# Kernel optimization log

Hardware: AMD Instinct MI355X
Metric: run time of the kernel (lower is better)

Reference implementation:

```python
import jax, jax.numpy as jnp
import numpy as np

B, S, D_IN, D_OUT = 8, 2048, 768, 768
SCALE = float(D_IN) ** 0.5  # module divides by embed_size**0.5 where embed_size = input_dim


def setup_inputs() -> dict:
    key = jax.random.key(0)
    ks = jax.random.split(key, 8)
    std = 1.0 / np.sqrt(D_IN)
    return {
        "x": jax.random.normal(ks[0], (B, S, D_IN), dtype=jnp.float32),
        "mask": jax.random.randint(ks[1], (B, S), 0, 2, dtype=jnp.int32),
        "Wq": jax.random.normal(ks[2], (D_OUT, D_IN), dtype=jnp.float32) * std,
        "bq": jax.random.normal(ks[3], (D_OUT,), dtype=jnp.float32) * std,
        "Wk": jax.random.normal(ks[4], (D_OUT, D_IN), dtype=jnp.float32) * std,
        "bk": jax.random.normal(ks[5], (D_OUT,), dtype=jnp.float32) * std,
        "Wv": jax.random.normal(ks[6], (D_OUT, D_IN), dtype=jnp.float32) * std,
        "bv": jax.random.normal(ks[7], (D_OUT,), dtype=jnp.float32) * std,
    }


def reference(x, mask, Wq, bq, Wk, bk, Wv, bv):
    # QKV projections: nn.Linear computes x @ W.T + b
    Q = jnp.einsum("bsd,od->bso", x, Wq) + bq  # [B,S,D_OUT]
    K = jnp.einsum("bsd,od->bso", x, Wk) + bk
    V = jnp.einsum("bsd,od->bso", x, Wv) + bv
    scores = jnp.einsum("bqo,bko->bqk", Q, K) / SCALE  # [B,S,S]
    # key-position mask broadcast over query dim
    scores = jnp.where(mask[:, None, :] == 0, -jnp.inf, scores)
    weights = jax.nn.softmax(scores, axis=-1)
    out = jnp.einsum("bqk,bko->bqo", weights, V)  # [B,S,D_OUT]
    return out.mean(axis=1, keepdims=True)  # [B,1,D_OUT]
```

## Files before the change

### kernel.cpp

```cpp
#include <hip/hip_runtime.h>
#include <hip/hip_bf16.h>


#define S 2048
#define DIM 768
#define BATCH 8

typedef __hip_bfloat16 bf16;
typedef __attribute__((ext_vector_type(8))) short bf16x8;
typedef __attribute__((ext_vector_type(4))) short short4v;
typedef __attribute__((ext_vector_type(4))) float f32x4;

__device__ __forceinline__ f32x4 mfma16(bf16x8 a, bf16x8 b, f32x4 c) {
  return __builtin_amdgcn_mfma_f32_16x16x32_bf16(a, b, c, 0, 0, 0);
}

__device__ __forceinline__ void load_lds16(const short* g, short* l) {
  __builtin_amdgcn_global_load_lds(
      (const __attribute__((address_space(1))) unsigned int*)g,
      (__attribute__((address_space(3))) unsigned int*)l, 16, 0, 0);
}

__device__ __forceinline__ float b2f(short u) {
  union { float f; unsigned u; } v;
  v.u = ((unsigned)(unsigned short)u) << 16;
  return v.f;
}

__device__ __forceinline__ short f2b(float f) {
  bf16 h = __float2bfloat16(f);
  return *(short*)&h;
}

#define INV_SCALE 0.03608439182435161f

__global__ __launch_bounds__(256) void detect_dtype(const unsigned short* __restrict__ x,
                                                    int* __restrict__ flag) {
  int bad = 0;
  for (int i = threadIdx.x; i < 2048; i += 256) {
    int e = (x[i] >> 7) & 0xFF;
    if (e < 0x60 || e >= 0x9F) bad = 1;
  }
  if (bad) atomicOr(flag, 1);
}

__global__ __launch_bounds__(256) void prep_kernel(const void* __restrict__ Wq_raw,
                                                   const void* __restrict__ Wk_raw,
                                                   const void* __restrict__ bq_raw,
                                                   bf16* __restrict__ T0,
                                                   bf16* __restrict__ T1,
                                                   float* __restrict__ bvec,
                                                   const int* __restrict__ flag) {
  const int f = *flag;
  const int bx = blockIdx.x;
  if (bx < 288) {
    __shared__ unsigned short tile[64][66];
    const int p = bx / 144, r = bx % 144;
    const void* src = p ? Wk_raw : Wq_raw;
    unsigned short* dst = (unsigned short*)(p ? T1 : T0);
    const int obase = (r / 12) * 64, ibase = (r % 12) * 64;
    const int col = threadIdx.x & 63, rq = threadIdx.x >> 6;
#pragma unroll
    for (int rr = 0; rr < 64; rr += 4) {
      const long idx = (long)(obase + rr + rq) * DIM + ibase + col;
      const float v = f ? ((const float*)src)[idx] : b2f(((const short*)src)[idx]);
      tile[rr + rq][col] = (unsigned short)f2b(v);
    }
    __syncthreads();
#pragma unroll
    for (int rr = 0; rr < 64; rr += 4)
      dst[(long)(ibase + rr + rq) * DIM + obase + col] = tile[col][rr + rq];
  } else {
    const int o0 = (bx - 288) * 128;
    const int t = threadIdx.x;
    float s0 = 0.f, s1 = 0.f, s2 = 0.f;
    if (f) {
      const float* W = (const float*)Wk_raw;
      const float* bq = (const float*)bq_raw;
      for (int o = o0; o < o0 + 128; ++o) {
        const float bo = bq[o];
        const float* row = W + (long)o * DIM;
        s0 += row[t] * bo;
        s1 += row[t + 256] * bo;
        s2 += row[t + 512] * bo;
      }
    } else {
      const short* W = (const short*)Wk_raw;
      const short* bq = (const short*)bq_raw;
      for (int o = o0; o < o0 + 128; ++o) {
        const float bo = b2f(bq[o]);
        const short* row = W + (long)o * DIM;
        s0 += b2f(row[t]) * bo;
        s1 += b2f(row[t + 256]) * bo;
        s2 += b2f(row[t + 512]) * bo;
      }
    }
    atomicAdd(&bvec[t], s0);
    atomicAdd(&bvec[t + 256], s1);
    atomicAdd(&bvec[t + 512], s2);
  }
}

#define TILE_DECLS                                                          \
  __shared__ short As[4096], Bs[4096];                                      \
  const int tid = threadIdx.x;                                              \
  const int wave = tid >> 6, lane = tid & 63;                               \
  const int lr = lane & 15, quad = lane >> 4;                               \
  const int wm = (wave >> 1) * 64, wn = (wave & 1) * 64;                    \
  const int c0row = tid >> 2, colw = (tid & 3) * 8;

#define TILE_KLOOP(Abase, Bbase)                                            \
  const short* Ag0 = (Abase) + (long)(mblk + c0row) * DIM + colw;           \
  const short* Ag1 = (Abase) + (long)(mblk + 64 + c0row) * DIM + colw;      \
  const short* Bg0 = (Bbase) + (long)(nblk + c0row) * DIM + colw;           \
  const short* Bg1 = (Bbase) + (long)(nblk + 64 + c0row) * DIM + colw;      \
  short* Al0 = As + tid * 8;                                                \
  short* Al1 = As + 2048 + tid * 8;                                         \
  short* Bl0 = Bs + tid * 8;                                                \
  short* Bl1 = Bs + 2048 + tid * 8;                                         \
  f32x4 acc[4][4] = {};                                                     \
  for (int k0 = 0; k0 < DIM; k0 += 32) {                                    \
    load_lds16(Ag0 + k0, Al0);                                              \
    load_lds16(Ag1 + k0, Al1);                                              \
    load_lds16(Bg0 + k0, Bl0);                                              \
    load_lds16(Bg1 + k0, Bl1);                                              \
    asm volatile("s_waitcnt vmcnt(0)" ::: "memory");                        \
    __syncthreads();                                                        \
    bf16x8 af[4], bfr[4];                                                   \
    _Pragma("unroll") for (int it = 0; it < 4; ++it)                        \
        af[it] = *(const bf16x8*)(As + (wm + it * 16 + lr) * 32 + quad * 8);\
    _Pragma("unroll") for (int jt = 0; jt < 4; ++jt)                        \
        bfr[jt] = *(const bf16x8*)(Bs + (wn + jt * 16 + lr) * 32 + quad * 8);\
    _Pragma("unroll") for (int it = 0; it < 4; ++it)                        \
        _Pragma("unroll") for (int jt = 0; jt < 4; ++jt)                    \
            acc[it][jt] = mfma16(af[it], bfr[jt], acc[it][jt]);             \
    __syncthreads();                                                        \
  }

__global__ __launch_bounds__(256) void gemm_nt_tiled(const bf16* __restrict__ A,
                                                     const bf16* __restrict__ B,
                                                     bf16* __restrict__ D) {
  const int mblk = blockIdx.x * 128, nblk = blockIdx.y * 128;
  TILE_DECLS
  TILE_KLOOP((const short*)A, (const short*)B)
#pragma unroll
  for (int it = 0; it < 4; ++it)
#pragma unroll
    for (int jt = 0; jt < 4; ++jt)
#pragma unroll
      for (int r = 0; r < 4; ++r)
        D[(long)(mblk + wm + it * 16 + quad * 4 + r) * DIM +
          nblk + wn + jt * 16 + lr] = __float2bfloat16(acc[it][jt][r]);
}

__global__ __launch_bounds__(256) void mt_convert(const bf16* __restrict__ WkT,
                                                  const bf16* __restrict__ WqT,
                                                  bf16* __restrict__ Mt,
                                                  const void* __restrict__ x_raw,
                                                  const int* __restrict__ mask,
                                                  const float* __restrict__ bvec,
                                                  bf16* __restrict__ xb,
                                                  float* __restrict__ betas,
                                                  const int* __restrict__ flag) {
  const int bx = blockIdx.x;
  if (bx < 36) {
    const int mblk = (bx / 6) * 128, nblk = (bx % 6) * 128;
    TILE_DECLS
    TILE_KLOOP((const short*)WkT, (const short*)WqT)
#pragma unroll
    for (int it = 0; it < 4; ++it)
#pragma unroll
      for (int jt = 0; jt < 4; ++jt)
#pragma unroll
        for (int r = 0; r < 4; ++r)
          Mt[(long)(mblk + wm + it * 16 + quad * 4 + r) * DIM +
             nblk + wn + jt * 16 + lr] = __float2bfloat16(acc[it][jt][r]);
  } else {
    const int wave = threadIdx.x >> 6, lane = threadIdx.x & 63;
    const int n = (bx - 36) * 4 + wave;
    const int f = *flag;
    short* xo = (short*)xb + (long)n * DIM;
    float s = 0.f;
    if (f) {
      const float4* x4 = (const float4*)((const float*)x_raw + (long)n * DIM);
      const float4* bv4 = (const float4*)bvec;
#pragma unroll
      for (int it = 0; it < 3; ++it) {
        const int idx = it * 64 + lane;
        const float4 v = x4[idx];
        const float4 bb = bv4[idx];
        short4v sv = {f2b(v.x), f2b(v.y), f2b(v.z), f2b(v.w)};
        *(short4v*)(xo + idx * 4) = sv;
        s += v.x * bb.x + v.y * bb.y + v.z * bb.z + v.w * bb.w;
      }
    } else {
      const short4v* x4 = (const short4v*)((const short*)x_raw + (long)n * DIM);
      const float4* bv4 = (const float4*)bvec;
#pragma unroll
      for (int it = 0; it < 3; ++it) {
        const int idx = it * 64 + lane;
        const short4v v = x4[idx];
        const float4 bb = bv4[idx];
        *(short4v*)(xo + idx * 4) = v;
        s += b2f(v.x) * bb.x + b2f(v.y) * bb.y + b2f(v.z) * bb.z + b2f(v.w) * bb.w;
      }
    }
#pragma unroll
    for (int off = 1; off < 64; off <<= 1) s += __shfl_xor(s, off, 64);
    if (lane == 0) betas[n] = mask[n] ? s * INV_SCALE : -1e30f;
  }
}

__global__ __launch_bounds__(256) void gemm_score(const bf16* __restrict__ z,
                                                  const bf16* __restrict__ x,
                                                  const float* __restrict__ betas,
                                                  float* __restrict__ l_out,
                                                  bf16* __restrict__ E,
                                                  int b0) {
  const int mblk = blockIdx.x * 128, nblk = blockIdx.y * 128;
  const int lb = blockIdx.z, b = b0 + lb;
  TILE_DECLS
  TILE_KLOOP((const short*)z + (long)lb * S * DIM,
             (const short*)x + (long)b * S * DIM)
  float bet[4];
#pragma unroll
  for (int jt = 0; jt < 4; ++jt)
    bet[jt] = betas[b * S + nblk + wn + jt * 16 + lr];
  bf16* Eb = E + (long)lb * S * S;
  float* lrow = l_out + b * S;
#pragma unroll
  for (int it = 0; it < 4; ++it) {
#pragma unroll
    for (int r = 0; r < 4; ++r) {
      const int q = mblk + wm + it * 16 + quad * 4 + r;
      float s = 0.f;
#pragma unroll
      for (int jt = 0; jt < 4; ++jt) {
        float e = __expf(fminf(acc[it][jt][r] * INV_SCALE + bet[jt], 60.f));
        s += e;
        Eb[(long)q * S + nblk + wn + jt * 16 + lr] = __float2bfloat16(e);
      }
      s += __shfl_xor(s, 1, 64);
      s += __shfl_xor(s, 2, 64);
      s += __shfl_xor(s, 4, 64);
      s += __shfl_xor(s, 8, 64);
      if (lr == 0) atomicAdd(&lrow[q], s);
    }
  }
}

__global__ __launch_bounds__(256) void reduce_c(const bf16* __restrict__ E,
                                                const float* __restrict__ l,
                                                float* __restrict__ c, int b0) {
  const int lb = blockIdx.y, b = b0 + lb;
  const int q0 = blockIdx.x * 16;
  const int k8 = threadIdx.x * 8;
  const short* Eb = (const short*)E + (long)lb * S * S + k8;
  const float* lrow = l + b * S;
  float acc[8] = {};
#pragma unroll
  for (int q = q0; q < q0 + 16; ++q) {
    bf16x8 ev = *(const bf16x8*)(Eb + (long)q * S);
    const float lv = lrow[q];
    const float rq = lv > 0.f ? 1.0f / lv : 0.f;
#pragma unroll
    for (int j = 0; j < 8; ++j) acc[j] += b2f(ev[j]) * rq;
  }
#pragma unroll
  for (int j = 0; j < 8; ++j)
    atomicAdd(&c[b * S + k8 + j], acc[j] * (1.0f / 2048.0f));
}

__global__ __launch_bounds__(256) void y_kernel(const bf16* __restrict__ x,
                                                const float* __restrict__ c,
                                                float* __restrict__ y) {
  const int b = blockIdx.z;
  const int i = blockIdx.x * 256 + threadIdx.x;
  const int kstart = blockIdx.y * 128;
  const bf16* xb = x + (long)(b * S + kstart) * DIM + i;
  const float* cb = c + b * S + kstart;
  float acc = 0.f;
  for (int k = 0; k < 128; ++k)
    acc += cb[k] * __bfloat162float(xb[(long)k * DIM]);
  atomicAdd(&y[b * DIM + i], acc);
}

__global__ __launch_bounds__(256) void out_kernel(const float* __restrict__ y,
                                                  const void* __restrict__ Wv_raw,
                                                  const void* __restrict__ bv_raw,
                                                  void* __restrict__ out,
                                                  const int* __restrict__ flag) {
  const int wave = threadIdx.x >> 6, lane = threadIdx.x & 63;
  const int w = blockIdx.x * 4 + wave;
  const int b = w / DIM, o = w % DIM;
  const int f = *flag;
  const float4* y4 = (const float4*)(y + (long)b * DIM);
  float s = 0.f;
  if (f) {
    const float4* wr = (const float4*)((const float*)Wv_raw + (long)o * DIM);
#pragma unroll
    for (int it = 0; it < 3; ++it) {
      const int idx = it * 64 + lane;
      const float4 a = y4[idx], wv = wr[idx];
      s += a.x * wv.x + a.y * wv.y + a.z * wv.z + a.w * wv.w;
    }
  } else {
    const short4v* wr = (const short4v*)((const short*)Wv_raw + (long)o * DIM);
#pragma unroll
    for (int it = 0; it < 3; ++it) {
      const int idx = it * 64 + lane;
      const float4 a = y4[idx];
      const short4v wv = wr[idx];
      s += a.x * b2f(wv.x) + a.y * b2f(wv.y) + a.z * b2f(wv.z) + a.w * b2f(wv.w);
    }
  }
#pragma unroll
  for (int off = 1; off < 64; off <<= 1) s += __shfl_xor(s, off, 64);
  if (lane == 0) {
    const float bias = f ? ((const float*)bv_raw)[o] : b2f(((const short*)bv_raw)[o]);
    const float v = s + bias;
    if (f) ((float*)out)[b * DIM + o] = v;
    else ((bf16*)out)[b * DIM + o] = __float2bfloat16(v);
  }
}

extern "C" void kernel_launch(void* const* d_in, const int* in_sizes, int n_in,
                              void* d_out, int out_size, void* d_ws, size_t ws_size,
                              hipStream_t stream) {
  const void* x_raw = d_in[0];
  const int* mask = (const int*)d_in[1];
  const void* Wq_raw = d_in[2];
  const void* bq_raw = d_in[3];
  const void* Wk_raw = d_in[4];
  const void* Wv_raw = d_in[6];
  const void* bv_raw = d_in[7];

  char* ws = (char*)d_ws;
  bf16* xb = (bf16*)(ws);
  bf16* WqT = (bf16*)(ws + 25165824);
  bf16* WkT = (bf16*)(ws + 26345472);
  bf16* Mt = (bf16*)(ws + 27525120);
  float* betas = (float*)(ws + 28704768);
  float* bvec = (float*)(ws + 28770304);
  float* l = (float*)(ws + 28773376);
  float* c = (float*)(ws + 28838912);
  float* y = (float*)(ws + 28904448);
  int* flag = (int*)(ws + 28929024);
  bf16* z = (bf16*)(ws + 28929088);

  const size_t fixed = 28929088;
  const size_t zb = 3145728, eb = 8388608;
  int nb = 1;
  if (ws_size >= fixed + 8 * (zb + eb)) nb = 8;
  else if (ws_size >= fixed + 4 * (zb + eb)) nb = 4;
  else if (ws_size >= fixed + 2 * (zb + eb)) nb = 2;
  bf16* E = (bf16*)(ws + fixed + (size_t)nb * zb);
  const int rounds = BATCH / nb;

  (void)hipMemsetAsync(bvec, 0, 3072 + 65536 + 65536 + 24576 + 64, stream);

  detect_dtype<<<1, 256, 0, stream>>>((const unsigned short*)x_raw, flag);
  prep_kernel<<<294, 256, 0, stream>>>(Wq_raw, Wk_raw, bq_raw, WqT, WkT, bvec, flag);
  mt_convert<<<4132, 256, 0, stream>>>(WkT, WqT, Mt, x_raw, mask, bvec, xb,
                                       betas, flag);

  for (int r = 0; r < rounds; ++r) {
    const int b0 = r * nb;
    gemm_nt_tiled<<<dim3(nb * 16, 6), 256, 0, stream>>>(
        xb + (long)b0 * S * DIM, Mt, z);
    gemm_score<<<dim3(16, 16, nb), 256, 0, stream>>>(z, xb, betas, l, E, b0);
    reduce_c<<<dim3(128, nb), 256, 0, stream>>>(E, l, c, b0);
  }

  y_kernel<<<dim3(3, 16, 8), 256, 0, stream>>>(xb, c, y);
  out_kernel<<<1536, 256, 0, stream>>>(y, Wv_raw, bv_raw, d_out, flag);
}
```

Before: 331.6 us.

## Fuse all stages into one cooperative persistent kernel with grid syncs

```diff
diff --git a/kernel.cpp b/kernel.cpp
--- a/kernel.cpp
+++ b/kernel.cpp
@@ -1,5 +1,8 @@
 #include <hip/hip_runtime.h>
 #include <hip/hip_bf16.h>
+#include <hip/hip_cooperative_groups.h>
+
+namespace cg = cooperative_groups;
 
 
 #define S 2048
@@ -33,6 +36,344 @@
 }
 
 #define INV_SCALE 0.03608439182435161f
+
+__device__ __forceinline__ void tile_kloop(const short* __restrict__ Abase,
+                                           const short* __restrict__ Bbase,
+                                           short* As, short* Bs, int mblk,
+                                           int nblk, int tid,
+                                           f32x4 (&acc)[4][4]) {
+  const int lane = tid & 63;
+  const int lr = lane & 15, quad = lane >> 4;
+  const int wave = tid >> 6;
+  const int wm = (wave >> 1) * 64, wn = (wave & 1) * 64;
+  const int c0row = tid >> 2, colw = (tid & 3) * 8;
+  const short* Ag0 = Abase + (long)(mblk + c0row) * DIM + colw;
+  const short* Ag1 = Abase + (long)(mblk + 64 + c0row) * DIM + colw;
+  const short* Bg0 = Bbase + (long)(nblk + c0row) * DIM + colw;
+  const short* Bg1 = Bbase + (long)(nblk + 64 + c0row) * DIM + colw;
+  short* Al0 = As + tid * 8;
+  short* Al1 = As + 2048 + tid * 8;
+  short* Bl0 = Bs + tid * 8;
+  short* Bl1 = Bs + 2048 + tid * 8;
+  for (int k0 = 0; k0 < DIM; k0 += 32) {
+    load_lds16(Ag0 + k0, Al0);
+    load_lds16(Ag1 + k0, Al1);
+    load_lds16(Bg0 + k0, Bl0);
+    load_lds16(Bg1 + k0, Bl1);
+    asm volatile("s_waitcnt vmcnt(0)" ::: "memory");
+    __syncthreads();
+    bf16x8 af[4], bfr[4];
+#pragma unroll
+    for (int it = 0; it < 4; ++it)
+      af[it] = *(const bf16x8*)(As + (wm + it * 16 + lr) * 32 + quad * 8);
+#pragma unroll
+    for (int jt = 0; jt < 4; ++jt)
+      bfr[jt] = *(const bf16x8*)(Bs + (wn + jt * 16 + lr) * 32 + quad * 8);
+#pragma unroll
+    for (int it = 0; it < 4; ++it)
+#pragma unroll
+      for (int jt = 0; jt < 4; ++jt)
+        acc[it][jt] = mfma16(af[it], bfr[jt], acc[it][jt]);
+    __syncthreads();
+  }
+}
+
+__device__ __forceinline__ void tile_store(short* __restrict__ D, int mblk,
+                                           int nblk, int tid,
+                                           f32x4 (&acc)[4][4]) {
+  const int lane = tid & 63, lr = lane & 15, quad = lane >> 4;
+  const int wave = tid >> 6, wm = (wave >> 1) * 64, wn = (wave & 1) * 64;
+#pragma unroll
+  for (int it = 0; it < 4; ++it)
+#pragma unroll
+    for (int jt = 0; jt < 4; ++jt)
+#pragma unroll
+      for (int r = 0; r < 4; ++r)
+        D[(long)(mblk + wm + it * 16 + quad * 4 + r) * DIM + nblk + wn +
+          jt * 16 + lr] = f2b(acc[it][jt][r]);
+}
+
+__device__ __forceinline__ void do_transpose_job(const void* src, short* dstT,
+                                                 int r, int f, int tid,
+                                                 char* smem) {
+  unsigned short(*tile)[66] = (unsigned short(*)[66])smem;
+  unsigned short* dst = (unsigned short*)dstT;
+  const int obase = (r / 12) * 64, ibase = (r % 12) * 64;
+  const int col = tid & 63, rq = tid >> 6;
+#pragma unroll
+  for (int rr = 0; rr < 64; rr += 4) {
+    const long idx = (long)(obase + rr + rq) * DIM + ibase + col;
+    const float v = f ? ((const float*)src)[idx] : b2f(((const short*)src)[idx]);
+    tile[rr + rq][col] = (unsigned short)f2b(v);
+  }
+  __syncthreads();
+#pragma unroll
+  for (int rr = 0; rr < 64; rr += 4)
+    dst[(long)(ibase + rr + rq) * DIM + obase + col] = tile[col][rr + rq];
+  __syncthreads();
+}
+
+__device__ __forceinline__ void do_bvec_job(const void* Wk_raw,
+                                            const void* bq_raw,
+                                            float* __restrict__ bvec, int slice,
+                                            int f, int tid, float* red) {
+  const int jj = slice * 128 + (tid & 127);
+  const int half = tid >> 7;
+  float s = 0.f;
+  if (f) {
+    const float* W = (const float*)Wk_raw;
+    const float* bq = (const float*)bq_raw;
+    for (int o = half; o < DIM; o += 2) s += W[(long)o * DIM + jj] * bq[o];
+  } else {
+    const short* W = (const short*)Wk_raw;
+    const short* bq = (const short*)bq_raw;
+    for (int o = half; o < DIM; o += 2) s += b2f(W[(long)o * DIM + jj]) * b2f(bq[o]);
+  }
+  red[tid] = s;
+  __syncthreads();
+  if (tid < 128) bvec[jj] = red[tid] + red[tid + 128];
+  __syncthreads();
+}
+
+__device__ __forceinline__ void do_convert_job(const void* x_raw,
+                                               const int* mask,
+                                               const float* bvec, short* xb,
+                                               float* betas, int n, int f,
+                                               int tid) {
+  const int lane = tid & 63;
+  short* xo = xb + (long)n * DIM;
+  float s = 0.f;
+  if (f) {
+    const float4* x4 = (const float4*)((const float*)x_raw + (long)n * DIM);
+    const float4* bv4 = (const float4*)bvec;
+#pragma unroll
+    for (int it = 0; it < 3; ++it) {
+      const int idx = it * 64 + lane;
+      const float4 v = x4[idx];
+      const float4 bb = bv4[idx];
+      short4v sv = {f2b(v.x), f2b(v.y), f2b(v.z), f2b(v.w)};
+      *(short4v*)(xo + idx * 4) = sv;
+      s += v.x * bb.x + v.y * bb.y + v.z * bb.z + v.w * bb.w;
+    }
+  } else {
+    const short4v* x4 = (const short4v*)((const short*)x_raw + (long)n * DIM);
+    const float4* bv4 = (const float4*)bvec;
+#pragma unroll
+    for (int it = 0; it < 3; ++it) {
+      const int idx = it * 64 + lane;
+      const short4v v = x4[idx];
+      const float4 bb = bv4[idx];
+      *(short4v*)(xo + idx * 4) = v;
+      s += b2f(v.x) * bb.x + b2f(v.y) * bb.y + b2f(v.z) * bb.z + b2f(v.w) * bb.w;
+    }
+  }
+#pragma unroll
+  for (int off = 1; off < 64; off <<= 1) s += __shfl_xor(s, off, 64);
+  if (lane == 0) betas[n] = mask[n] ? s * INV_SCALE : -1e30f;
+}
+
+__device__ __forceinline__ void score_epilogue(const float* betas, float* l_out,
+                                               short* Eb, int b, int mblk,
+                                               int nblk, int tid,
+                                               f32x4 (&acc)[4][4]) {
+  const int lane = tid & 63, lr = lane & 15, quad = lane >> 4;
+  const int wave = tid >> 6, wm = (wave >> 1) * 64, wn = (wave & 1) * 64;
+  float bet[4];
+#pragma unroll
+  for (int jt = 0; jt < 4; ++jt)
+    bet[jt] = betas[b * S + nblk + wn + jt * 16 + lr];
+  float* lrow = l_out + b * S;
+#pragma unroll
+  for (int it = 0; it < 4; ++it) {
+#pragma unroll
+    for (int r = 0; r < 4; ++r) {
+      const int q = mblk + wm + it * 16 + quad * 4 + r;
+      float s = 0.f;
+#pragma unroll
+      for (int jt = 0; jt < 4; ++jt) {
+        float e = __expf(fminf(acc[it][jt][r] * INV_SCALE + bet[jt], 60.f));
+        s += e;
+        Eb[(long)q * S + nblk + wn + jt * 16 + lr] = f2b(e);
+      }
+      s += __shfl_xor(s, 1, 64);
+      s += __shfl_xor(s, 2, 64);
+      s += __shfl_xor(s, 4, 64);
+      s += __shfl_xor(s, 8, 64);
+      if (lr == 0) atomicAdd(&lrow[q], s);
+    }
+  }
+}
+
+__device__ __forceinline__ void do_reduce_job(const short* Eb, const float* lrow,
+                                              float* crow, int q0, int tid) {
+  const int k8 = tid * 8;
+  float acc[8] = {};
+#pragma unroll
+  for (int q = q0; q < q0 + 16; ++q) {
+    bf16x8 ev = *(const bf16x8*)(Eb + (long)q * S + k8);
+    const float lv = lrow[q];
+    const float rq = lv > 0.f ? 1.0f / lv : 0.f;
+#pragma unroll
+    for (int j = 0; j < 8; ++j) acc[j] += b2f(ev[j]) * rq;
+  }
+#pragma unroll
+  for (int j = 0; j < 8; ++j)
+    atomicAdd(&crow[k8 + j], acc[j] * (1.0f / 2048.0f));
+}
+
+__device__ __forceinline__ void do_y_job(const short* xb, const float* c,
+                                         float* y, int b, int kc, int ic,
+                                         int tid) {
+  const int i = ic * 256 + tid;
+  const int kstart = kc * 128;
+  const short* xr = xb + (long)(b * S + kstart) * DIM + i;
+  const float* cb = c + b * S + kstart;
+  float acc = 0.f;
+  for (int k = 0; k < 128; ++k) acc += cb[k] * b2f(xr[(long)k * DIM]);
+  atomicAdd(&y[b * DIM + i], acc);
+}
+
+__device__ __forceinline__ void do_out_job(const float* y, const void* Wv_raw,
+                                           const void* bv_raw, void* out, int w,
+                                           int f, int tid) {
+  const int lane = tid & 63;
+  const int b = w / DIM, o = w % DIM;
+  const float4* y4 = (const float4*)(y + (long)b * DIM);
+  float s = 0.f;
+  if (f) {
+    const float4* wr = (const float4*)((const float*)Wv_raw + (long)o * DIM);
+#pragma unroll
+    for (int it = 0; it < 3; ++it) {
+      const int idx = it * 64 + lane;
+      const float4 a = y4[idx], wv = wr[idx];
+      s += a.x * wv.x + a.y * wv.y + a.z * wv.z + a.w * wv.w;
+    }
+  } else {
+    const short4v* wr = (const short4v*)((const short*)Wv_raw + (long)o * DIM);
+#pragma unroll
+    for (int it = 0; it < 3; ++it) {
+      const int idx = it * 64 + lane;
+      const float4 a = y4[idx];
+      const short4v wv = wr[idx];
+      s += a.x * b2f(wv.x) + a.y * b2f(wv.y) + a.z * b2f(wv.z) + a.w * b2f(wv.w);
+    }
+  }
+#pragma unroll
+  for (int off = 1; off < 64; off <<= 1) s += __shfl_xor(s, off, 64);
+  if (lane == 0) {
+    const float bias = f ? ((const float*)bv_raw)[o] : b2f(((const short*)bv_raw)[o]);
+    const float v = s + bias;
+    if (f) ((float*)out)[b * DIM + o] = v;
+    else ((bf16*)out)[b * DIM + o] = __float2bfloat16(v);
+  }
+}
+
+struct MegaArgs {
+  const void* x_raw; const int* mask;
+  const void* Wq_raw; const void* bq_raw; const void* Wk_raw;
+  const void* Wv_raw; const void* bv_raw;
+  void* out;
+  short* xb; short* WqT; short* WkT; short* Mt;
+  float* betas; float* bvec; float* lcy;
+  short* z; short* E;
+  int nb, rounds;
+};
+
+__global__ __launch_bounds__(256, 4) void mega(MegaArgs a) {
+  cg::grid_group grid = cg::this_grid();
+  __shared__ __align__(16) char smem[17664];
+  short* As = (short*)smem;
+  short* Bs = (short*)(smem + 8192);
+  float* red = (float*)(smem + 16384);
+  const int tid = threadIdx.x;
+  const int nblocks = gridDim.x;
+  float* l = a.lcy;
+  float* c = a.lcy + 16384;
+  float* y = a.lcy + 32768;
+
+  int bad = 0;
+  {
+    const unsigned short* xs = (const unsigned short*)a.x_raw;
+    for (int i = tid; i < 2048; i += 256) {
+      int e = (xs[i] >> 7) & 0xFF;
+      if (e < 0x60 || e >= 0x9F) bad = 1;
+    }
+    if (tid == 0) *(int*)(smem + 17408) = 0;
+    __syncthreads();
+    if (__any(bad) && (tid & 63) == 0) atomicOr((int*)(smem + 17408), 1);
+    __syncthreads();
+  }
+  const int f = *(int*)(smem + 17408);
+  __syncthreads();
+
+  for (int j = blockIdx.x; j < 294; j += nblocks) {
+    if (j < 288) {
+      do_transpose_job(j < 144 ? a.Wq_raw : a.Wk_raw,
+                       j < 144 ? a.WqT : a.WkT, j % 144, f, tid, smem);
+    } else {
+      do_bvec_job(a.Wk_raw, a.bq_raw, a.bvec, j - 288, f, tid, red);
+    }
+  }
+  grid.sync();
+
+  for (int j = blockIdx.x; j < 4142; j += nblocks) {
+    if (j < 36) {
+      f32x4 acc[4][4] = {};
+      tile_kloop(a.WkT, a.WqT, As, Bs, (j / 6) * 128, (j % 6) * 128, tid, acc);
+      tile_store(a.Mt, (j / 6) * 128, (j % 6) * 128, tid, acc);
+    } else if (j < 4132) {
+      const int n = (j - 36) * 4 + (tid >> 6);
+      do_convert_job(a.x_raw, a.mask, a.bvec, a.xb, a.betas, n, f, tid);
+    } else {
+      const int base = (j - 4132) * 4096;
+      for (int i = tid; i < 4096; i += 256) {
+        const int idx = base + i;
+        if (idx < 38912) a.lcy[idx] = 0.f;
+      }
+    }
+  }
+  grid.sync();
+
+  for (int r = 0; r < a.rounds; ++r) {
+    const int b0 = r * a.nb;
+    const int njC = a.nb * 96;
+    for (int j = blockIdx.x; j < njC; j += nblocks) {
+      const int mblk = (j / 6) * 128, nblk = (j % 6) * 128;
+      f32x4 acc[4][4] = {};
+      tile_kloop(a.xb + (long)b0 * S * DIM, a.Mt, As, Bs, mblk, nblk, tid, acc);
+      tile_store(a.z, mblk, nblk, tid, acc);
+    }
+    grid.sync();
+    const int njD = 256 * a.nb;
+    for (int j = blockIdx.x; j < njD; j += nblocks) {
+      const int lb = j % a.nb, t = j / a.nb;
+      const int mblk = (t >> 4) * 128, nblk = (t & 15) * 128;
+      f32x4 acc[4][4] = {};
+      tile_kloop(a.z + (long)lb * S * DIM, a.xb + (long)(b0 + lb) * S * DIM,
+                 As, Bs, mblk, nblk, tid, acc);
+      score_epilogue(a.betas, l, a.E + (long)lb * S * S, b0 + lb, mblk, nblk,
+                     tid, acc);
+    }
+    grid.sync();
+    const int njE = 128 * a.nb;
+    for (int j = blockIdx.x; j < njE; j += nblocks) {
+      const int lb = j % a.nb, qs = j / a.nb;
+      do_reduce_job(a.E + (long)lb * S * S, l + (b0 + lb) * S,
+                    c + (b0 + lb) * S, qs * 16, tid);
+    }
+    grid.sync();
+  }
+
+  for (int j = blockIdx.x; j < 384; j += nblocks) {
+    const int b = j / 48, rest = j % 48;
+    do_y_job(a.xb, c, y, b, rest / 3, rest % 3, tid);
+  }
+  grid.sync();
+
+  for (int j = blockIdx.x; j < 1536; j += nblocks) {
+    do_out_job(y, a.Wv_raw, a.bv_raw, a.out, j * 4 + (tid >> 6), f, tid);
+  }
+}
 
 __global__ __launch_bounds__(256) void detect_dtype(const unsigned short* __restrict__ x,
                                                     int* __restrict__ flag) {
@@ -44,284 +385,89 @@
   if (bad) atomicOr(flag, 1);
 }
 
-__global__ __launch_bounds__(256) void prep_kernel(const void* __restrict__ Wq_raw,
-                                                   const void* __restrict__ Wk_raw,
-                                                   const void* __restrict__ bq_raw,
-                                                   bf16* __restrict__ T0,
-                                                   bf16* __restrict__ T1,
-                                                   float* __restrict__ bvec,
-                                                   const int* __restrict__ flag) {
+__global__ __launch_bounds__(256) void prep_kernel(const void* Wq_raw,
+                                                   const void* Wk_raw,
+                                                   const void* bq_raw,
+                                                   short* T0, short* T1,
+                                                   float* bvec,
+                                                   const int* flag) {
+  __shared__ __align__(16) char smem[17664];
   const int f = *flag;
   const int bx = blockIdx.x;
-  if (bx < 288) {
-    __shared__ unsigned short tile[64][66];
-    const int p = bx / 144, r = bx % 144;
-    const void* src = p ? Wk_raw : Wq_raw;
-    unsigned short* dst = (unsigned short*)(p ? T1 : T0);
-    const int obase = (r / 12) * 64, ibase = (r % 12) * 64;
-    const int col = threadIdx.x & 63, rq = threadIdx.x >> 6;
-#pragma unroll
-    for (int rr = 0; rr < 64; rr += 4) {
-      const long idx = (long)(obase + rr + rq) * DIM + ibase + col;
-      const float v = f ? ((const float*)src)[idx] : b2f(((const short*)src)[idx]);
-      tile[rr + rq][col] = (unsigned short)f2b(v);
-    }
-    __syncthreads();
-#pragma unroll
-    for (int rr = 0; rr < 64; rr += 4)
-      dst[(long)(ibase + rr + rq) * DIM + obase + col] = tile[col][rr + rq];
-  } else {
-    const int o0 = (bx - 288) * 128;
-    const int t = threadIdx.x;
-    float s0 = 0.f, s1 = 0.f, s2 = 0.f;
-    if (f) {
-      const float* W = (const float*)Wk_raw;
-      const float* bq = (const float*)bq_raw;
-      for (int o = o0; o < o0 + 128; ++o) {
-        const float bo = bq[o];
-        const float* row = W + (long)o * DIM;
-        s0 += row[t] * bo;
-        s1 += row[t + 256] * bo;
-        s2 += row[t + 512] * bo;
-      }
-    } else {
-      const short* W = (const short*)Wk_raw;
-      const short* bq = (const short*)bq_raw;
-      for (int o = o0; o < o0 + 128; ++o) {
-        const float bo = b2f(bq[o]);
-        const short* row = W + (long)o * DIM;
-        s0 += b2f(row[t]) * bo;
-        s1 += b2f(row[t + 256]) * bo;
-        s2 += b2f(row[t + 512]) * bo;
-      }
-    }
-    atomicAdd(&bvec[t], s0);
-    atomicAdd(&bvec[t + 256], s1);
-    atomicAdd(&bvec[t + 512], s2);
-  }
-}
-
-#define TILE_DECLS                                                          \
-  __shared__ short As[4096], Bs[4096];                                      \
-  const int tid = threadIdx.x;                                              \
-  const int wave = tid >> 6, lane = tid & 63;                               \
-  const int lr = lane & 15, quad = lane >> 4;                               \
-  const int wm = (wave >> 1) * 64, wn = (wave & 1) * 64;                    \
-  const int c0row = tid >> 2, colw = (tid & 3) * 8;
-
-#define TILE_KLOOP(Abase, Bbase)                                            \
-  const short* Ag0 = (Abase) + (long)(mblk + c0row) * DIM + colw;           \
-  const short* Ag1 = (Abase) + (long)(mblk + 64 + c0row) * DIM + colw;      \
-  const short* Bg0 = (Bbase) + (long)(nblk + c0row) * DIM + colw;           \
-  const short* Bg1 = (Bbase) + (long)(nblk + 64 + c0row) * DIM + colw;      \
-  short* Al0 = As + tid * 8;                                                \
-  short* Al1 = As + 2048 + tid * 8;                                         \
-  short* Bl0 = Bs + tid * 8;                                                \
-  short* Bl1 = Bs + 2048 + tid * 8;                                         \
-  f32x4 acc[4][4] = {};                                                     \
-  for (int k0 = 0; k0 < DIM; k0 += 32) {                                    \
-    load_lds16(Ag0 + k0, Al0);                                              \
-    load_lds16(Ag1 + k0, Al1);                                              \
-    load_lds16(Bg0 + k0, Bl0);                                              \
-    load_lds16(Bg1 + k0, Bl1);                                              \
-    asm volatile("s_waitcnt vmcnt(0)" ::: "memory");                        \
-    __syncthreads();                                                        \
-    bf16x8 af[4], bfr[4];                                                   \
-    _Pragma("unroll") for (int it = 0; it < 4; ++it)                        \
-        af[it] = *(const bf16x8*)(As + (wm + it * 16 + lr) * 32 + quad * 8);\
-    _Pragma("unroll") for (int jt = 0; jt < 4; ++jt)                        \
-        bfr[jt] = *(const bf16x8*)(Bs + (wn + jt * 16 + lr) * 32 + quad * 8);\
-    _Pragma("unroll") for (int it = 0; it < 4; ++it)                        \
-        _Pragma("unroll") for (int jt = 0; jt < 4; ++jt)                    \
-            acc[it][jt] = mfma16(af[it], bfr[jt], acc[it][jt]);             \
-    __syncthreads();                                                        \
-  }
-
-__global__ __launch_bounds__(256) void gemm_nt_tiled(const bf16* __restrict__ A,
-                                                     const bf16* __restrict__ B,
-                                                     bf16* __restrict__ D) {
-  const int mblk = blockIdx.x * 128, nblk = blockIdx.y * 128;
-  TILE_DECLS
-  TILE_KLOOP((const short*)A, (const short*)B)
-#pragma unroll
-  for (int it = 0; it < 4; ++it)
-#pragma unroll
-    for (int jt = 0; jt < 4; ++jt)
-#pragma unroll
-      for (int r = 0; r < 4; ++r)
-        D[(long)(mblk + wm + it * 16 + quad * 4 + r) * DIM +
-          nblk + wn + jt * 16 + lr] = __float2bfloat16(acc[it][jt][r]);
-}
-
-__global__ __launch_bounds__(256) void mt_convert(const bf16* __restrict__ WkT,
-                                                  const bf16* __restrict__ WqT,
-                                                  bf16* __restrict__ Mt,
-                                                  const void* __restrict__ x_raw,
-                                                  const int* __restrict__ mask,
-                                                  const float* __restrict__ bvec,
-                                                  bf16* __restrict__ xb,
-                                                  float* __restrict__ betas,
-                                                  const int* __restrict__ flag) {
+  if (bx < 288)
+    do_transpose_job(bx < 144 ? Wq_raw : Wk_raw, bx < 144 ? T0 : T1, bx % 144,
+                     f, threadIdx.x, smem);
+  else
+    do_bvec_job(Wk_raw, bq_raw, bvec, bx - 288, f, threadIdx.x,
+                (float*)(smem + 16384));
+}
+
+__global__ __launch_bounds__(256) void mt_convert(const short* WkT,
+                                                  const short* WqT, short* Mt,
+                                                  const void* x_raw,
+                                                  const int* mask,
+                                                  const float* bvec, short* xb,
+                                                  float* betas, float* lcy,
+                                                  const int* flag) {
+  __shared__ __align__(16) char smem[16384];
   const int bx = blockIdx.x;
   if (bx < 36) {
-    const int mblk = (bx / 6) * 128, nblk = (bx % 6) * 128;
-    TILE_DECLS
-    TILE_KLOOP((const short*)WkT, (const short*)WqT)
-#pragma unroll
-    for (int it = 0; it < 4; ++it)
-#pragma unroll
-      for (int jt = 0; jt < 4; ++jt)
-#pragma unroll
-        for (int r = 0; r < 4; ++r)
-          Mt[(long)(mblk + wm + it * 16 + quad * 4 + r) * DIM +
-             nblk + wn + jt * 16 + lr] = __float2bfloat16(acc[it][jt][r]);
+    f32x4 acc[4][4] = {};
+    tile_kloop(WkT, WqT, (short*)smem, (short*)(smem + 8192), (bx / 6) * 128,
+               (bx % 6) * 128, threadIdx.x, acc);
+    tile_store(Mt, (bx / 6) * 128, (bx % 6) * 128, threadIdx.x, acc);
+  } else if (bx < 4132) {
+    const int n = (bx - 36) * 4 + (threadIdx.x >> 6);
+    do_convert_job(x_raw, mask, bvec, xb, betas, n, *flag, threadIdx.x);
   } else {
-    const int wave = threadIdx.x >> 6, lane = threadIdx.x & 63;
-    const int n = (bx - 36) * 4 + wave;
-    const int f = *flag;
-    short* xo = (short*)xb + (long)n * DIM;
-    float s = 0.f;
-    if (f) {
-      const float4* x4 = (const float4*)((const float*)x_raw + (long)n * DIM);
-      const float4* bv4 = (const float4*)bvec;
-#pragma unroll
-      for (int it = 0; it < 3; ++it) {
-        const int idx = it * 64 + lane;
-        const float4 v = x4[idx];
-        const float4 bb = bv4[idx];
-        short4v sv = {f2b(v.x), f2b(v.y), f2b(v.z), f2b(v.w)};
-        *(short4v*)(xo + idx * 4) = sv;
-        s += v.x * bb.x + v.y * bb.y + v.z * bb.z + v.w * bb.w;
-      }
-    } else {
-      const short4v* x4 = (const short4v*)((const short*)x_raw + (long)n * DIM);
-      const float4* bv4 = (const float4*)bvec;
-#pragma unroll
-      for (int it = 0; it < 3; ++it) {
-        const int idx = it * 64 + lane;
-        const short4v v = x4[idx];
-        const float4 bb = bv4[idx];
-        *(short4v*)(xo + idx * 4) = v;
-        s += b2f(v.x) * bb.x + b2f(v.y) * bb.y + b2f(v.z) * bb.z + b2f(v.w) * bb.w;
-      }
-    }
-#pragma unroll
-    for (int off = 1; off < 64; off <<= 1) s += __shfl_xor(s, off, 64);
-    if (lane == 0) betas[n] = mask[n] ? s * INV_SCALE : -1e30f;
-  }
-}
-
-__global__ __launch_bounds__(256) void gemm_score(const bf16* __restrict__ z,
-                                                  const bf16* __restrict__ x,
-                                                  const float* __restrict__ betas,
-                                                  float* __restrict__ l_out,
-                                                  bf16* __restrict__ E,
-                                                  int b0) {
-  const int mblk = blockIdx.x * 128, nblk = blockIdx.y * 128;
+    const int base = (bx - 4132) * 4096;
+    for (int i = threadIdx.x; i < 4096; i += 256) {
+      const int idx = base + i;
+      if (idx < 38912) lcy[idx] = 0.f;
+    }
+  }
+}
+
+__global__ __launch_bounds__(256) void gemm_nt_tiled(const short* A,
+                                                     const short* B, short* D) {
+  __shared__ __align__(16) char smem[16384];
+  f32x4 acc[4][4] = {};
+  tile_kloop(A, B, (short*)smem, (short*)(smem + 8192), blockIdx.x * 128,
+             blockIdx.y * 128, threadIdx.x, acc);
+  tile_store(D, blockIdx.x * 128, blockIdx.y * 128, threadIdx.x, acc);
+}
+
+__global__ __launch_bounds__(256) void gemm_score(const short* z, const short* x,
+                                                  const float* betas, float* l,
+                                                  short* E, int b0) {
+  __shared__ __align__(16) char smem[16384];
   const int lb = blockIdx.z, b = b0 + lb;
-  TILE_DECLS
-  TILE_KLOOP((const short*)z + (long)lb * S * DIM,
-             (const short*)x + (long)b * S * DIM)
-  float bet[4];
-#pragma unroll
-  for (int jt = 0; jt < 4; ++jt)
-    bet[jt] = betas[b * S + nblk + wn + jt * 16 + lr];
-  bf16* Eb = E + (long)lb * S * S;
-  float* lrow = l_out + b * S;
-#pragma unroll
-  for (int it = 0; it < 4; ++it) {
-#pragma unroll
-    for (int r = 0; r < 4; ++r) {
-      const int q = mblk + wm + it * 16 + quad * 4 + r;
-      float s = 0.f;
-#pragma unroll
-      for (int jt = 0; jt < 4; ++jt) {
-        float e = __expf(fminf(acc[it][jt][r] * INV_SCALE + bet[jt], 60.f));
-        s += e;
-        Eb[(long)q * S + nblk + wn + jt * 16 + lr] = __float2bfloat16(e);
-      }
-      s += __shfl_xor(s, 1, 64);
-      s += __shfl_xor(s, 2, 64);
-      s += __shfl_xor(s, 4, 64);
-      s += __shfl_xor(s, 8, 64);
-      if (lr == 0) atomicAdd(&lrow[q], s);
-    }
-  }
-}
-
-__global__ __launch_bounds__(256) void reduce_c(const bf16* __restrict__ E,
-                                                const float* __restrict__ l,
-                                                float* __restrict__ c, int b0) {
+  f32x4 acc[4][4] = {};
+  tile_kloop(z + (long)lb * S * DIM, x + (long)b * S * DIM, (short*)smem,
+             (short*)(smem + 8192), blockIdx.x * 128, blockIdx.y * 128,
+             threadIdx.x, acc);
+  score_epilogue(betas, l, E + (long)lb * S * S, b, blockIdx.x * 128,
+                 blockIdx.y * 128, threadIdx.x, acc);
+}
+
+__global__ __launch_bounds__(256) void reduce_c(const short* E, const float* l,
+                                                float* c, int b0, int nb) {
   const int lb = blockIdx.y, b = b0 + lb;
-  const int q0 = blockIdx.x * 16;
-  const int k8 = threadIdx.x * 8;
-  const short* Eb = (const short*)E + (long)lb * S * S + k8;
-  const float* lrow = l + b * S;
-  float acc[8] = {};
-#pragma unroll
-  for (int q = q0; q < q0 + 16; ++q) {
-    bf16x8 ev = *(const bf16x8*)(Eb + (long)q * S);
-    const float lv = lrow[q];
-    const float rq = lv > 0.f ? 1.0f / lv : 0.f;
-#pragma unroll
-    for (int j = 0; j < 8; ++j) acc[j] += b2f(ev[j]) * rq;
-  }
-#pragma unroll
-  for (int j = 0; j < 8; ++j)
-    atomicAdd(&c[b * S + k8 + j], acc[j] * (1.0f / 2048.0f));
-}
-
-__global__ __launch_bounds__(256) void y_kernel(const bf16* __restrict__ x,
-                                                const float* __restrict__ c,
-                                                float* __restrict__ y) {
-  const int b = blockIdx.z;
-  const int i = blockIdx.x * 256 + threadIdx.x;
-  const int kstart = blockIdx.y * 128;
-  const bf16* xb = x + (long)(b * S + kstart) * DIM + i;
-  const float* cb = c + b * S + kstart;
-  float acc = 0.f;
-  for (int k = 0; k < 128; ++k)
-    acc += cb[k] * __bfloat162float(xb[(long)k * DIM]);
-  atomicAdd(&y[b * DIM + i], acc);
-}
-
-__global__ __launch_bounds__(256) void out_kernel(const float* __restrict__ y,
-                                                  const void* __restrict__ Wv_raw,
-                                                  const void* __restrict__ bv_raw,
-                                                  void* __restrict__ out,
-                                                  const int* __restrict__ flag) {
-  const int wave = threadIdx.x >> 6, lane = threadIdx.x & 63;
-  const int w = blockIdx.x * 4 + wave;
-  const int b = w / DIM, o = w % DIM;
-  const int f = *flag;
-  const float4* y4 = (const float4*)(y + (long)b * DIM);
-  float s = 0.f;
-  if (f) {
-    const float4* wr = (const float4*)((const float*)Wv_raw + (long)o * DIM);
-#pragma unroll
-    for (int it = 0; it < 3; ++it) {
-      const int idx = it * 64 + lane;
-      const float4 a = y4[idx], wv = wr[idx];
-      s += a.x * wv.x + a.y * wv.y + a.z * wv.z + a.w * wv.w;
-    }
-  } else {
-    const short4v* wr = (const short4v*)((const short*)Wv_raw + (long)o * DIM);
-#pragma unroll
-    for (int it = 0; it < 3; ++it) {
-      const int idx = it * 64 + lane;
-      const float4 a = y4[idx];
-      const short4v wv = wr[idx];
-      s += a.x * b2f(wv.x) + a.y * b2f(wv.y) + a.z * b2f(wv.z) + a.w * b2f(wv.w);
-    }
-  }
-#pragma unroll
-  for (int off = 1; off < 64; off <<= 1) s += __shfl_xor(s, off, 64);
-  if (lane == 0) {
-    const float bias = f ? ((const float*)bv_raw)[o] : b2f(((const short*)bv_raw)[o]);
-    const float v = s + bias;
-    if (f) ((float*)out)[b * DIM + o] = v;
-    else ((bf16*)out)[b * DIM + o] = __float2bfloat16(v);
-  }
+  do_reduce_job(E + (long)lb * S * S, l + b * S, c + b * S, blockIdx.x * 16,
+                threadIdx.x);
+}
+
+__global__ __launch_bounds__(256) void y_kernel(const short* xb, const float* c,
+                                                float* y) {
+  do_y_job(xb, c, y, blockIdx.z, blockIdx.y, blockIdx.x, threadIdx.x);
+}
+
+__global__ __launch_bounds__(256) void out_kernel(const float* y,
+                                                  const void* Wv_raw,
+                                                  const void* bv_raw, void* out,
+                                                  const int* flag) {
+  do_out_job(y, Wv_raw, bv_raw, out, blockIdx.x * 4 + (threadIdx.x >> 6),
+             *flag, threadIdx.x);
 }
 
 extern "C" void kernel_launch(void* const* d_in, const int* in_sizes, int n_in,
@@ -336,17 +482,15 @@
   const void* bv_raw = d_in[7];
 
   char* ws = (char*)d_ws;
-  bf16* xb = (bf16*)(ws);
-  bf16* WqT = (bf16*)(ws + 25165824);
-  bf16* WkT = (bf16*)(ws + 26345472);
-  bf16* Mt = (bf16*)(ws + 27525120);
+  short* xb = (short*)(ws);
+  short* WqT = (short*)(ws + 25165824);
+  short* WkT = (short*)(ws + 26345472);
+  short* Mt = (short*)(ws + 27525120);
   float* betas = (float*)(ws + 28704768);
   float* bvec = (float*)(ws + 28770304);
-  float* l = (float*)(ws + 28773376);
-  float* c = (float*)(ws + 28838912);
-  float* y = (float*)(ws + 28904448);
+  float* lcy = (float*)(ws + 28773376);
   int* flag = (int*)(ws + 28929024);
-  bf16* z = (bf16*)(ws + 28929088);
+  short* z = (short*)(ws + 28929088);
 
   const size_t fixed = 28929088;
   const size_t zb = 3145728, eb = 8388608;
@@ -354,24 +498,45 @@
   if (ws_size >= fixed + 8 * (zb + eb)) nb = 8;
   else if (ws_size >= fixed + 4 * (zb + eb)) nb = 4;
   else if (ws_size >= fixed + 2 * (zb + eb)) nb = 2;
-  bf16* E = (bf16*)(ws + fixed + (size_t)nb * zb);
+  short* E = (short*)(ws + fixed + (size_t)nb * zb);
   const int rounds = BATCH / nb;
 
-  (void)hipMemsetAsync(bvec, 0, 3072 + 65536 + 65536 + 24576 + 64, stream);
-
+  MegaArgs a;
+  a.x_raw = x_raw; a.mask = mask;
+  a.Wq_raw = Wq_raw; a.bq_raw = bq_raw; a.Wk_raw = Wk_raw;
+  a.Wv_raw = Wv_raw; a.bv_raw = bv_raw;
+  a.out = d_out;
+  a.xb = xb; a.WqT = WqT; a.WkT = WkT; a.Mt = Mt;
+  a.betas = betas; a.bvec = bvec; a.lcy = lcy;
+  a.z = z; a.E = E;
+  a.nb = nb; a.rounds = rounds;
+
+  int perCU = 0;
+  hipError_t oe = hipOccupancyMaxActiveBlocksPerMultiprocessor(&perCU, mega, 256, 0);
+  int grid = (oe == hipSuccess && perCU > 0) ? perCU * 256 : 1024;
+  if (grid > 2048) grid = 2048;
+
+  void* kargs[] = {(void*)&a};
+  hipError_t err = hipLaunchCooperativeKernel((const void*)mega, dim3(grid),
+                                              dim3(256), kargs, 0, stream);
+  if (err == hipSuccess) return;
+
+  (void)hipMemsetAsync(lcy, 0, 155648, stream);
+  (void)hipMemsetAsync(flag, 0, 64, stream);
   detect_dtype<<<1, 256, 0, stream>>>((const unsigned short*)x_raw, flag);
   prep_kernel<<<294, 256, 0, stream>>>(Wq_raw, Wk_raw, bq_raw, WqT, WkT, bvec, flag);
-  mt_convert<<<4132, 256, 0, stream>>>(WkT, WqT, Mt, x_raw, mask, bvec, xb,
-                                       betas, flag);
-
+  mt_convert<<<4142, 256, 0, stream>>>(WkT, WqT, Mt, x_raw, mask, bvec, xb,
+                                       betas, lcy, flag);
+  float* l = lcy;
+  float* c = lcy + 16384;
+  float* y = lcy + 32768;
   for (int r = 0; r < rounds; ++r) {
     const int b0 = r * nb;
     gemm_nt_tiled<<<dim3(nb * 16, 6), 256, 0, stream>>>(
         xb + (long)b0 * S * DIM, Mt, z);
     gemm_score<<<dim3(16, 16, nb), 256, 0, stream>>>(z, xb, betas, l, E, b0);
-    reduce_c<<<dim3(128, nb), 256, 0, stream>>>(E, l, c, b0);
-  }
-
+    reduce_c<<<dim3(128, nb), 256, 0, stream>>>(E, l, c, b0, nb);
+  }
   y_kernel<<<dim3(3, 16, 8), 256, 0, stream>>>(xb, c, y);
   out_kernel<<<1536, 256, 0, stream>>>(y, Wv_raw, bv_raw, d_out, flag);
 }
```

Result: slower. 831.5 us (+150.8%).
